# Performance work log

Hardware: AMD Instinct MI355X
Metric: run time of the kernel (lower is better)

Reference implementation:

```python
import jax, jax.numpy as jnp
import numpy as np

B, N, S, K, D = 16, 4096, 1024, 32, 64
MLP = (64, 64, 128)
EPS = 1e-5  # BatchNorm2d default eps


def setup_inputs() -> dict:
    key = jax.random.key(0)
    ks = jax.random.split(key, 16)
    inp = {
        'xyz': jax.random.normal(ks[0], (B, N, 3), dtype=jnp.float32),
        'normals': jax.random.normal(ks[1], (B, N, 3), dtype=jnp.float32),
        'points': jax.random.normal(ks[2], (B, N, D), dtype=jnp.float32),
        'fps_idx': jax.random.randint(ks[3], (B, S), 0, N),
    }
    last = D
    for i, c in enumerate(MLP):
        inp[f'w{i}'] = jax.random.normal(ks[4 + i], (c, last), dtype=jnp.float32) * (1.0 / np.sqrt(last))
        inp[f'b{i}'] = jnp.zeros((c,), dtype=jnp.float32)
        inp[f'g{i}'] = jnp.ones((c,), dtype=jnp.float32)
        inp[f'bt{i}'] = jnp.zeros((c,), dtype=jnp.float32)
        last = c
    return inp


def _group(points, idx):
    # points: [B,N,C], idx: [B,S,K] -> [B,S,K,C]
    b, s, k = idx.shape
    flat = idx.reshape(b, s * k)
    g = jnp.take_along_axis(points, flat[:, :, None], axis=1)
    return g.reshape(b, s, k, points.shape[-1])


def _forward(xyz, normals, points, fps_idx, params):
    new_xyz = jnp.take_along_axis(xyz, fps_idx[:, :, None], axis=1)        # [B,S,3]
    new_normals = jnp.take_along_axis(normals, fps_idx[:, :, None], axis=1)
    # squared distances [B,S,N] (algebraic form of the broadcasted cdist)
    d = (jnp.sum(new_xyz ** 2, -1)[:, :, None]
         + jnp.sum(xyz ** 2, -1)[:, None, :]
         - 2.0 * jnp.einsum('bsc,bnc->bsn', new_xyz, xyz))
    _, idx = jax.lax.top_k(-d, K)                                          # K nearest
    x = _group(points, idx)                                                # [B,S,K,D]
    x = jnp.transpose(x, (0, 3, 2, 1))                                     # [B,D,K,S]
    for (w, b, g, bt) in params:
        x = jnp.einsum('oc,bcks->boks', w, x) + b[None, :, None, None]     # 1x1 conv
        m = jnp.mean(x, axis=(0, 2, 3), keepdims=True)                     # BN (batch stats)
        v = jnp.var(x, axis=(0, 2, 3), keepdims=True)
        x = (x - m) * jax.lax.rsqrt(v + EPS) * g[None, :, None, None] + bt[None, :, None, None]
        x = jax.nn.relu(x)
    feat = jnp.transpose(jnp.max(x, axis=2), (0, 2, 1))                    # [B,S,C_out]
    return new_xyz, new_normals, feat, fps_idx


def reference(xyz, normals, points, fps_idx,
              w0, b0, g0, bt0, w1, b1, g1, bt1, w2, b2, g2, bt2):
    params = ((w0, b0, g0, bt0), (w1, b1, g1, bt1), (w2, b2, g2, bt2))
    return _forward(xyz, normals, points, fps_idx, params)
```

## Files before the change

kernel.cpp:

```cpp
#include <hip/hip_runtime.h>
#include <hip/hip_bf16.h>

#define B_ 16
#define N_ 4096
#define S_ 1024
#define K_ 32
#define D_ 64
#define M_ (B_*S_*K_)
#define EPS_ 1e-5f

#define OUT_NRM  (B_*S_*3)
#define OUT_FEAT (2*B_*S_*3)
#define OUT_FPS  (OUT_FEAT + B_*S_*128)

typedef __attribute__((ext_vector_type(8))) short bf16x8;
typedef __attribute__((ext_vector_type(4))) float f32x4;
typedef unsigned long long u64;

__device__ __forceinline__ unsigned short rnb(float x){
  return (unsigned short)((__float_as_uint(x) + 0x8000u) >> 16);
}
__device__ __forceinline__ void split1(float x, short& h, short& l){
  unsigned ux = __float_as_uint(x);
  unsigned uh = (ux + 0x8000u) & 0xFFFF0000u;
  h = (short)(uh >> 16);
  float lo = x - __uint_as_float(uh);
  l = (short)((__float_as_uint(lo) + 0x8000u) >> 16);
}
__device__ __forceinline__ unsigned f2key(float d){
  unsigned u = __float_as_uint(d);
  return u ^ ((unsigned)(((int)u) >> 31) | 0x80000000u);
}
__device__ __forceinline__ float key2f(unsigned u){
  unsigned v = (u & 0x80000000u) ? (u ^ 0x80000000u) : ~u;
  return __uint_as_float(v);
}
__device__ __forceinline__ unsigned mprefix(u64 m){
  return __builtin_amdgcn_mbcnt_hi((unsigned)(m >> 32),
         __builtin_amdgcn_mbcnt_lo((unsigned)m, 0u));
}

__device__ __forceinline__ float hred4_sum(const float v[4], int l){
  bool hi8 = (l & 8) != 0;
  float send0 = hi8 ? v[0] : v[2];
  float send1 = hi8 ? v[1] : v[3];
  float r0 = __shfl_xor(send0, 8);
  float r1 = __shfl_xor(send1, 8);
  float a0 = (hi8 ? v[2] : v[0]) + r0;
  float a1 = (hi8 ? v[3] : v[1]) + r1;
  bool hi4 = (l & 4) != 0;
  float send = hi4 ? a0 : a1;
  float r = __shfl_xor(send, 4);
  float a = (hi4 ? a1 : a0) + r;
  a += __shfl_xor(a, 2);
  a += __shfl_xor(a, 1);
  return a;
}
__device__ __forceinline__ float hred4_max(const float v[4], int l){
  bool hi8 = (l & 8) != 0;
  float send0 = hi8 ? v[0] : v[2];
  float send1 = hi8 ? v[1] : v[3];
  float r0 = __shfl_xor(send0, 8);
  float r1 = __shfl_xor(send1, 8);
  float a0 = fmaxf(hi8 ? v[2] : v[0], r0);
  float a1 = fmaxf(hi8 ? v[3] : v[1], r1);
  bool hi4 = (l & 4) != 0;
  float send = hi4 ? a0 : a1;
  float r = __shfl_xor(send, 4);
  float a = fmaxf(hi4 ? a1 : a0, r);
  a = fmaxf(a, __shfl_xor(a, 2));
  a = fmaxf(a, __shfl_xor(a, 1));
  return a;
}

__global__ void prep_kernel(const float* __restrict__ xyz, const float* __restrict__ nrm,
                            const int* __restrict__ fps,
                            const float* __restrict__ w0, const float* __restrict__ w1,
                            const float* __restrict__ w2,
                            float* __restrict__ out, float4* __restrict__ px,
                            unsigned short* __restrict__ wdst, float* __restrict__ stats){
  const int bid = blockIdx.x, tid = threadIdx.x;
  if (bid < 256){
    int t = bid*256 + tid;
    const float* p = xyz + (size_t)t*3;
    float x = p[0], y = p[1], z = p[2];
    float pp = __fadd_rn(__fadd_rn(__fmul_rn(x,x), __fmul_rn(y,y)), __fmul_rn(z,z));
    px[t] = make_float4(x, y, z, pp);
  } else if (bid < 320){
    int t = (bid-256)*256 + tid;
    int b = t >> 10;
    int n = fps[t];
    const float* xp = xyz + ((size_t)b*N_ + n)*3;
    out[t*3+0] = xp[0]; out[t*3+1] = xp[1]; out[t*3+2] = xp[2];
    const float* pp = nrm + ((size_t)b*N_ + n)*3;
    out[OUT_NRM + t*3+0] = pp[0]; out[OUT_NRM + t*3+1] = pp[1]; out[OUT_NRM + t*3+2] = pp[2];
    out[OUT_FPS + t] = (float)n;
  } else if (bid < 384){
    int e = (bid-320)*256 + tid;
    const float* W; int base;
    if (e < 4096){ W = w0; base = 0; }
    else if (e < 8192){ W = w1; base = 4096; }
    else { W = w2; base = 8192; }
    int r = e - base;
    int frag = r >> 9;
    int lane = (r >> 3) & 63;
    int j = r & 7;
    int cht = frag >> 1, ks = frag & 1;
    int m = lane & 15, quad = lane >> 4;
    int ch = cht*16 + m, k = ks*32 + quad*8 + j;
    wdst[e] = rnb(W[ch*64 + k]);
  } else {
    stats[(bid-384)*256 + tid] = 0.f;
  }
}

#define DIST3(Q,P) __fsub_rn(__fadd_rn((Q).w,(P).w), __fmul_rn(2.f, \
  __fadd_rn(__fadd_rn(__fmul_rn((Q).x,(P).x), __fmul_rn((Q).y,(P).y)), __fmul_rn((Q).z,(P).z))))

#define RANKSTEP(KK,LO,HI) do{ \
  unsigned mid_ = (LO) + (((HI) - (LO)) >> 1); \
  u64 mm_ = __ballot((KK) <= mid_); \
  if (__popcll(mm_) >= 32) (HI) = mid_; else (LO) = mid_ + 1; \
}while(0)

#define SELFIN(KEY,PAIR,KV,OB) do{ \
  u64 mlt_ = __ballot((KEY) < (KV)); \
  int c1_ = __popcll(mlt_); \
  u64 meq_ = __ballot((KEY) == (KV)); \
  int need_ = 32 - c1_; \
  bool ineq_ = ((KEY) == (KV)); \
  bool seleq_; \
  if (__popcll(meq_) == need_){ seleq_ = ineq_; } \
  else { \
    unsigned myi_ = ineq_ ? (unsigned)((PAIR) & 0xFFFull) : 0xFFFFu; \
    unsigned li_ = 0, hii_ = 0xFFFu; \
    for (int it2_ = 0; it2_ < 12; ++it2_){ \
      unsigned mid_ = li_ + ((hii_ - li_) >> 1); \
      int c_ = __popcll(__ballot(myi_ <= mid_)); \
      if (c_ >= need_) hii_ = mid_; else li_ = mid_ + 1; \
    } \
    seleq_ = (myi_ <= li_); \
  } \
  if ((KEY) < (KV)) idxout[(OB) + mprefix(mlt_)] = (int)((PAIR) & 0xFFFull); \
  u64 msel_ = __ballot(seleq_); \
  if (seleq_) idxout[(OB) + c1_ + mprefix(msel_)] = (int)((PAIR) & 0xFFFull); \
}while(0)

__device__ __forceinline__ void sel_fallback(const u64* sp, unsigned tot, int l,
                                             int* __restrict__ outp){
  if (tot <= 64){
    u64 pair = sp[l];
    u64 plo = 0, phi = (1ull << 44) - 1;
    for (int it = 0; it < 44; ++it){
      u64 mid = plo + ((phi - plo) >> 1);
      u64 m = __ballot(pair <= mid);
      if (__popcll(m) >= 32) phi = mid; else plo = mid + 1;
    }
    bool sel = (pair <= plo);
    u64 m = __ballot(sel);
    unsigned pos = mprefix(m);
    if (sel) outp[pos] = (int)(pair & 0xFFFull);
  } else {
    u64 pa = sp[l], pb = sp[64 + l];
    u64 plo = 0, phi = (1ull << 44) - 1;
    for (int it = 0; it < 44; ++it){
      u64 mid = plo + ((phi - plo) >> 1);
      int c = __popcll(__ballot(pa <= mid)) + __popcll(__ballot(pb <= mid));
      if (c >= 32) phi = mid; else plo = mid + 1;
    }
    int ca = (pa <= plo) ? 1 : 0;
    int cb = (pb <= plo) ? 1 : 0;
    int c2 = ca + cb, inc = c2;
    #pragma unroll
    for (int off = 1; off < 64; off <<= 1){
      int tv = __shfl_up(inc, off);
      if (l >= off) inc += tv;
    }
    int pos = inc - c2;
    if (ca){ outp[pos] = (int)(pa & 0xFFFull); pos++; }
    if (cb){ outp[pos] = (int)(pb & 0xFFFull); }
  }
}

__global__ __launch_bounds__(256, 8) void knn_kernel(const float4* __restrict__ pxyz,
                                                     const int* __restrict__ fps,
                                                     int* __restrict__ idxout){
  __shared__ u64 spair[4][2][128];
  __shared__ float4 stab[256];
  const int t = threadIdx.x, w = t >> 6, l = t & 63;
  const int b = blockIdx.x >> 7;
  const float4* __restrict__ Pp = pxyz + (size_t)b*N_;
  const int q0 = blockIdx.x*8 + w*2;
  const int nq0 = fps[q0], nq1 = fps[q0+1];
  const float4 Q0 = Pp[nq0], Q1 = Pp[nq1];

  float vmin0 = 3.0e38f, vmin1 = 3.0e38f;
  for (int ch = 0; ch < 16; ch++){
    __syncthreads();
    stab[t] = Pp[ch*256 + t];
    __syncthreads();
    #pragma unroll
    for (int j = 0; j < 4; j++){
      float4 P = stab[j*64 + l];
      float d0 = DIST3(Q0, P); vmin0 = fminf(vmin0, d0);
      float d1 = DIST3(Q1, P); vmin1 = fminf(vmin1, d1);
    }
  }

  unsigned a0 = f2key(vmin0), a1 = f2key(vmin1);
  unsigned tl0 = 0, th0 = 0xFFFFFFFFu, tl1 = 0, th1 = 0xFFFFFFFFu;
  for (int it = 0; it < 32; ++it){
    RANKSTEP(a0, tl0, th0);
    RANKSTEP(a1, tl1, th1);
  }
  const float T0 = key2f(tl0), T1 = key2f(tl1);

  spair[w][0][l] = ~0ull; spair[w][0][64 + l] = ~0ull;
  spair[w][1][l] = ~0ull; spair[w][1][64 + l] = ~0ull;

  unsigned cnt0 = 0, cnt1 = 0;
  for (int ch = 0; ch < 16; ch++){
    __syncthreads();
    stab[t] = Pp[ch*256 + t];
    __syncthreads();
    #pragma unroll
    for (int j = 0; j < 4; j++){
      unsigned n = (unsigned)(ch*256 + j*64 + l);
      float4 P = stab[j*64 + l];
      {
        float d = DIST3(Q0, P);
        bool c = (d <= T0);
        u64 m = __ballot(c);
        if (c){ unsigned pos = cnt0 + mprefix(m);
                if (pos < 128) spair[w][0][pos] = ((u64)f2key(d) << 12) | n; }
        cnt0 += (unsigned)__popcll(m);
      }
      {
        float d = DIST3(Q1, P);
        bool c = (d <= T1);
        u64 m = __ballot(c);
        if (c){ unsigned pos = cnt1 + mprefix(m);
                if (pos < 128) spair[w][1][pos] = ((u64)f2key(d) << 12) | n; }
        cnt1 += (unsigned)__popcll(m);
      }
    }
  }

  const size_t obase = (size_t)q0 * K_;
  if (cnt0 <= 64 && cnt1 <= 64){
    u64 P0 = spair[w][0][l], P1 = spair[w][1][l];
    unsigned K0 = (unsigned)(P0 >> 12), K1 = (unsigned)(P1 >> 12);
    unsigned s0l = 0, s0h = 0xFFFFFFFFu, s1l = 0, s1h = 0xFFFFFFFFu;
    for (int it = 0; it < 32; ++it){
      RANKSTEP(K0, s0l, s0h);
      RANKSTEP(K1, s1l, s1h);
    }
    SELFIN(K0, P0, s0l, obase);
    SELFIN(K1, P1, s1l, obase + K_);
  } else {
    sel_fallback(&spair[w][0][0], cnt0, l, idxout + obase);
    sel_fallback(&spair[w][1][0], cnt1, l, idxout + obase + K_);
  }
}

__global__ __launch_bounds__(256, 3) void conv1_mfma(const float* __restrict__ pts,
    const int* __restrict__ idx, const unsigned short* __restrict__ wpk,
    const float* __restrict__ bias, unsigned short* __restrict__ Yo,
    float* __restrict__ stats){
  __shared__ float sred[4][128];
  __shared__ uint4 Wl4[512];
  const unsigned short* Wl = (const unsigned short*)Wl4;
  const int t = threadIdx.x, w = t>>6, l = t&63, quad = l>>4, lr = l&15;
  const int m0 = blockIdx.x*256;
  const int Rw = m0 + w*64;
  const int b = m0 >> 15;
  Wl4[t] = ((const uint4*)wpk)[t];
  Wl4[256 + t] = ((const uint4*)wpk)[256 + t];
  f32x4 acc[4][4];
  #pragma unroll
  for (int c = 0; c < 4; c++)
    #pragma unroll
    for (int rt = 0; rt < 4; rt++)
      acc[c][rt] = (f32x4){0.f,0.f,0.f,0.f};
  int ri[4];
  #pragma unroll
  for (int rt = 0; rt < 4; rt++) ri[rt] = idx[Rw + rt*16 + lr];
  __syncthreads();
  #pragma unroll
  for (int s = 0; s < 2; s++){
    bf16x8 wfs[4];
    #pragma unroll
    for (int c = 0; c < 4; c++)
      wfs[c] = *(const bf16x8*)(Wl + (((c*2+s)<<6) + l)*8);
    #pragma unroll
    for (int rt = 0; rt < 4; rt++){
      const float* pr = pts + ((size_t)(b*4096 + ri[rt]))*64;
      float4 v0 = *(const float4*)(pr + s*32 + quad*8);
      float4 v1 = *(const float4*)(pr + s*32 + quad*8 + 4);
      float xs[8] = {v0.x,v0.y,v0.z,v0.w,v1.x,v1.y,v1.z,v1.w};
      bf16x8 xh, xl;
      #pragma unroll
      for (int j = 0; j < 8; j++){ short hh, ll; split1(xs[j], hh, ll); xh[j]=hh; xl[j]=ll; }
      #pragma unroll
      for (int c = 0; c < 4; c++){
        acc[c][rt] = __builtin_amdgcn_mfma_f32_16x16x32_bf16(wfs[c], xh, acc[c][rt], 0,0,0);
        acc[c][rt] = __builtin_amdgcn_mfma_f32_16x16x32_bf16(wfs[c], xl, acc[c][rt], 0,0,0);
      }
    }
  }
  const int rtg0 = Rw >> 4;
  #pragma unroll
  for (int c = 0; c < 4; c++){
    float4 bq = *(const float4*)(bias + c*16 + quad*4);
    float bqa[4] = {bq.x, bq.y, bq.z, bq.w};
    float sv[4] = {0,0,0,0}, qv[4] = {0,0,0,0};
    int kb = c*2 + (quad>>1);
    int sub = (quad&1)*4;
    #pragma unroll
    for (int rt = 0; rt < 4; rt++){
      float y[4];
      #pragma unroll
      for (int r = 0; r < 4; r++){
        y[r] = acc[c][rt][r] + bqa[r];
        sv[r] += y[r];
        qv[r] += y[r]*y[r];
      }
      uint2 p;
      p.x = (unsigned)rnb(y[0]) | ((unsigned)rnb(y[1])<<16);
      p.y = (unsigned)rnb(y[2]) | ((unsigned)rnb(y[3])<<16);
      *(uint2*)(Yo + ((((rtg0+rt)*8 + kb)*16 + lr)*8 + sub)) = p;
    }
    float S = hred4_sum(sv, l);
    float Q = hred4_sum(qv, l);
    if ((l & 3) == 0){
      int ch = c*16 + quad*4 + ((l>>3)&1)*2 + ((l>>2)&1);
      sred[w][ch] = S;
      sred[w][64 + ch] = Q;
    }
  }
  __syncthreads();
  if (t < 128){
    float tot = sred[0][t]+sred[1][t]+sred[2][t]+sred[3][t];
    unsafeAtomicAdd(&stats[(blockIdx.x & 7)*512 + t], tot);
  }
}

__global__ __launch_bounds__(256, 3) void conv2_mfma(const unsigned short* __restrict__ Yi,
    const unsigned short* __restrict__ wpk, const float* __restrict__ bias,
    const float* __restrict__ gg, const float* __restrict__ btv,
    unsigned short* __restrict__ Yo, float* __restrict__ stats){
  __shared__ float sred[4][128];
  __shared__ float sAff[128];
  __shared__ uint4 Wl4[512];
  const unsigned short* Wl = (const unsigned short*)Wl4;
  const int t = threadIdx.x, w = t>>6, l = t&63, quad = l>>4, lr = l&15;
  const int m0 = blockIdx.x*256;
  const int Rw = m0 + w*64;
  Wl4[t] = ((const uint4*)wpk)[t];
  Wl4[256 + t] = ((const uint4*)wpk)[256 + t];
  if (t < 64){
    const float inv = 1.f/(float)M_;
    float S = 0.f, Q = 0.f;
    #pragma unroll
    for (int r = 0; r < 8; r++){
      S += stats[r*512 + t];
      Q += stats[r*512 + 64 + t];
    }
    float mean = S * inv;
    float var  = Q * inv - mean*mean;
    float a = gg[t] * rsqrtf(var + EPS_);
    sAff[t] = a;
    sAff[64 + t] = btv[t] - mean*a;
  }
  f32x4 acc[4][4];
  #pragma unroll
  for (int c = 0; c < 4; c++)
    #pragma unroll
    for (int rt = 0; rt < 4; rt++)
      acc[c][rt] = (f32x4){0.f,0.f,0.f,0.f};
  const int rtg0 = Rw >> 4;
  uint4 u[2][4];
  #pragma unroll
  for (int s = 0; s < 2; s++)
    #pragma unroll
    for (int rt = 0; rt < 4; rt++)
      u[s][rt] = *(const uint4*)(Yi + (((rtg0+rt)*8 + s*4 + quad)*16 + lr)*8);
  __syncthreads();
  #pragma unroll
  for (int s = 0; s < 2; s++){
    float4 A0 = *(const float4*)(sAff + s*32 + quad*8);
    float4 A1 = *(const float4*)(sAff + s*32 + quad*8 + 4);
    float4 B0 = *(const float4*)(sAff + 64 + s*32 + quad*8);
    float4 B1 = *(const float4*)(sAff + 64 + s*32 + quad*8 + 4);
    float aA[8] = {A0.x,A0.y,A0.z,A0.w,A1.x,A1.y,A1.z,A1.w};
    float aB[8] = {B0.x,B0.y,B0.z,B0.w,B1.x,B1.y,B1.z,B1.w};
    bf16x8 wfs[4];
    #pragma unroll
    for (int c = 0; c < 4; c++)
      wfs[c] = *(const bf16x8*)(Wl + (((c*2+s)<<6) + l)*8);
    #pragma unroll
    for (int rt = 0; rt < 4; rt++){
      unsigned ua[4] = {u[s][rt].x, u[s][rt].y, u[s][rt].z, u[s][rt].w};
      bf16x8 xb;
      #pragma unroll
      for (int j = 0; j < 8; j++){
        unsigned wd = ua[j>>1];
        float yf = __uint_as_float((j&1) ? (wd & 0xFFFF0000u) : (wd << 16));
        float x = fmaxf(0.f, fmaf(yf, aA[j], aB[j]));
        xb[j] = (short)rnb(x);
      }
      #pragma unroll
      for (int c = 0; c < 4; c++)
        acc[c][rt] = __builtin_amdgcn_mfma_f32_16x16x32_bf16(wfs[c], xb, acc[c][rt], 0,0,0);
    }
  }
  #pragma unroll
  for (int c = 0; c < 4; c++){
    float4 bq = *(const float4*)(bias + c*16 + quad*4);
    float bqa[4] = {bq.x, bq.y, bq.z, bq.w};
    float sv[4] = {0,0,0,0}, qv[4] = {0,0,0,0};
    int kb = c*2 + (quad>>1);
    int sub = (quad&1)*4;
    #pragma unroll
    for (int rt = 0; rt < 4; rt++){
      float y[4];
      #pragma unroll
      for (int r = 0; r < 4; r++){
        y[r] = acc[c][rt][r] + bqa[r];
        sv[r] += y[r];
        qv[r] += y[r]*y[r];
      }
      uint2 p;
      p.x = (unsigned)rnb(y[0]) | ((unsigned)rnb(y[1])<<16);
      p.y = (unsigned)rnb(y[2]) | ((unsigned)rnb(y[3])<<16);
      *(uint2*)(Yo + ((((rtg0+rt)*8 + kb)*16 + lr)*8 + sub)) = p;
    }
    float S = hred4_sum(sv, l);
    float Q = hred4_sum(qv, l);
    if ((l & 3) == 0){
      int ch = c*16 + quad*4 + ((l>>3)&1)*2 + ((l>>2)&1);
      sred[w][ch] = S;
      sred[w][64 + ch] = Q;
    }
  }
  __syncthreads();
  if (t < 128){
    float tot = sred[0][t]+sred[1][t]+sred[2][t]+sred[3][t];
    unsafeAtomicAdd(&stats[(blockIdx.x & 7)*512 + 128 + t], tot);
  }
}

__global__ __launch_bounds__(256, 3) void conv3_mfma(const unsigned short* __restrict__ Yi,
    const unsigned short* __restrict__ wpk, const float* __restrict__ bias,
    const float* __restrict__ gg, const float* __restrict__ btv,
    float* __restrict__ ymax, float* __restrict__ stats){
  __shared__ float sred[4][256];
  __shared__ float sAff[128];
  __shared__ uint4 Wl4[1024];
  const unsigned short* Wl = (const unsigned short*)Wl4;
  const int t = threadIdx.x, w = t>>6, l = t&63, quad = l>>4, lr = l&15;
  const int m0 = blockIdx.x*128;
  const int Rw = m0 + w*32;
  #pragma unroll
  for (int i = 0; i < 4; i++) Wl4[i*256 + t] = ((const uint4*)wpk)[i*256 + t];
  if (t < 64){
    const float inv = 1.f/(float)M_;
    float S = 0.f, Q = 0.f;
    #pragma unroll
    for (int r = 0; r < 8; r++){
      S += stats[r*512 + 128 + t];
      Q += stats[r*512 + 192 + t];
    }
    float mean = S * inv;
    float var  = Q * inv - mean*mean;
    float a = gg[t] * rsqrtf(var + EPS_);
    sAff[t] = a;
    sAff[64 + t] = btv[t] - mean*a;
  }
  f32x4 acc[8][2];
  #pragma unroll
  for (int c = 0; c < 8; c++){
    acc[c][0] = (f32x4){0.f,0.f,0.f,0.f};
    acc[c][1] = (f32x4){0.f,0.f,0.f,0.f};
  }
  const int rtg0 = Rw >> 4;
  uint4 u[2][2];
  #pragma unroll
  for (int s = 0; s < 2; s++)
    #pragma unroll
    for (int rt = 0; rt < 2; rt++)
      u[s][rt] = *(const uint4*)(Yi + (((rtg0+rt)*8 + s*4 + quad)*16 + lr)*8);
  __syncthreads();
  #pragma unroll
  for (int s = 0; s < 2; s++){
    float4 A0 = *(const float4*)(sAff + s*32 + quad*8);
    float4 A1 = *(const float4*)(sAff + s*32 + quad*8 + 4);
    float4 B0 = *(const float4*)(sAff + 64 + s*32 + quad*8);
    float4 B1 = *(const float4*)(sAff + 64 + s*32 + quad*8 + 4);
    float aA[8] = {A0.x,A0.y,A0.z,A0.w,A1.x,A1.y,A1.z,A1.w};
    float aB[8] = {B0.x,B0.y,B0.z,B0.w,B1.x,B1.y,B1.z,B1.w};
    #pragma unroll
    for (int rt = 0; rt < 2; rt++){
      unsigned ua[4] = {u[s][rt].x, u[s][rt].y, u[s][rt].z, u[s][rt].w};
      bf16x8 xb;
      #pragma unroll
      for (int j = 0; j < 8; j++){
        unsigned wd = ua[j>>1];
        float yf = __uint_as_float((j&1) ? (wd & 0xFFFF0000u) : (wd << 16));
        float x = fmaxf(0.f, fmaf(yf, aA[j], aB[j]));
        xb[j] = (short)rnb(x);
      }
      #pragma unroll
      for (int c = 0; c < 8; c++){
        bf16x8 wfc = *(const bf16x8*)(Wl + (((c*2+s)<<6) + l)*8);
        acc[c][rt] = __builtin_amdgcn_mfma_f32_16x16x32_bf16(wfc, xb, acc[c][rt], 0,0,0);
      }
    }
  }
  const int g = Rw >> 5;
  #pragma unroll
  for (int c = 0; c < 8; c++){
    float4 bq = *(const float4*)(bias + c*16 + quad*4);
    float bqa[4] = {bq.x, bq.y, bq.z, bq.w};
    float sv[4], qv[4], mv[4];
    #pragma unroll
    for (int r = 0; r < 4; r++){
      float y0 = acc[c][0][r] + bqa[r];
      float y1 = acc[c][1][r] + bqa[r];
      sv[r] = y0 + y1;
      qv[r] = y0*y0 + y1*y1;
      mv[r] = fmaxf(y0, y1);
    }
    float S = hred4_sum(sv, l);
    float Q = hred4_sum(qv, l);
    float Mx = hred4_max(mv, l);
    if ((l & 3) == 0){
      int ch = c*16 + quad*4 + ((l>>3)&1)*2 + ((l>>2)&1);
      sred[w][ch] = S;
      sred[w][128 + ch] = Q;
      ymax[(size_t)g*128 + ch] = Mx;
    }
  }
  __syncthreads();
  {
    float tot = sred[0][t]+sred[1][t]+sred[2][t]+sred[3][t];
    unsafeAtomicAdd(&stats[(blockIdx.x & 7)*512 + 256 + t], tot);
  }
}

__global__ void final_kernel(const float* __restrict__ ymax,
                             const float* __restrict__ stats,
                             const float* __restrict__ gg, const float* __restrict__ btv,
                             float* __restrict__ out){
  __shared__ float sA[128], sB[128];
  const int tid = threadIdx.x;
  if (tid < 128){
    const float inv = 1.f/(float)M_;
    float S = 0.f, Q = 0.f;
    #pragma unroll
    for (int r = 0; r < 8; r++){
      S += stats[r*512 + 256 + tid];
      Q += stats[r*512 + 384 + tid];
    }
    float mean = S * inv;
    float var  = Q * inv - mean*mean;
    float a = gg[tid] * rsqrtf(var + EPS_);
    sA[tid] = a;
    sB[tid] = btv[tid] - mean*a;
  }
  __syncthreads();
  const size_t base = ((size_t)blockIdx.x*256 + tid)*8;
  float4 v0 = *(const float4*)(ymax + base);
  float4 v1 = *(const float4*)(ymax + base + 4);
  const int c0 = (int)(base & 127);
  float4 a0 = *(const float4*)(sA + c0);
  float4 a1 = *(const float4*)(sA + c0 + 4);
  float4 b0 = *(const float4*)(sB + c0);
  float4 b1 = *(const float4*)(sB + c0 + 4);
  float4 o0, o1;
  o0.x = fmaxf(0.f, a0.x*v0.x + b0.x); o0.y = fmaxf(0.f, a0.y*v0.y + b0.y);
  o0.z = fmaxf(0.f, a0.z*v0.z + b0.z); o0.w = fmaxf(0.f, a0.w*v0.w + b0.w);
  o1.x = fmaxf(0.f, a1.x*v1.x + b1.x); o1.y = fmaxf(0.f, a1.y*v1.y + b1.y);
  o1.z = fmaxf(0.f, a1.z*v1.z + b1.z); o1.w = fmaxf(0.f, a1.w*v1.w + b1.w);
  *(float4*)(out + OUT_FEAT + base) = o0;
  *(float4*)(out + OUT_FEAT + base + 4) = o1;
}

extern "C" void kernel_launch(void* const* d_in, const int* in_sizes, int n_in,
                              void* d_out, int out_size, void* d_ws, size_t ws_size,
                              hipStream_t stream) {
  const float* xyz = (const float*)d_in[0];
  const float* nrm = (const float*)d_in[1];
  const float* pts = (const float*)d_in[2];
  const int*   fps = (const int*)d_in[3];
  const float* w0  = (const float*)d_in[4];
  const float* b0  = (const float*)d_in[5];
  const float* g0  = (const float*)d_in[6];
  const float* bt0 = (const float*)d_in[7];
  const float* w1  = (const float*)d_in[8];
  const float* b1  = (const float*)d_in[9];
  const float* g1  = (const float*)d_in[10];
  const float* bt1 = (const float*)d_in[11];
  const float* w2  = (const float*)d_in[12];
  const float* b2  = (const float*)d_in[13];
  const float* g2  = (const float*)d_in[14];
  const float* bt2 = (const float*)d_in[15];
  float* out = (float*)d_out;

  char* ws = (char*)d_ws;
  float* stats = (float*)ws;
  int*   idxb  = (int*)(ws + 20480);
  float* ymax  = (float*)(ws + 2117632);
  float4* pxyz = (float4*)(ws + 10506240);
  unsigned short* wpack = (unsigned short*)(ws + 11554816);
  unsigned short* Y1 = (unsigned short*)(ws + 18878464);
  unsigned short* Y2 = (unsigned short*)(ws + 85987328);

  prep_kernel<<<400, 256, 0, stream>>>(xyz, nrm, fps, w0, w1, w2, out, pxyz, wpack, stats);
  knn_kernel<<<2048, 256, 0, stream>>>(pxyz, fps, idxb);
  conv1_mfma<<<2048, 256, 0, stream>>>(pts, idxb, wpack, b0, Y1, stats);
  conv2_mfma<<<2048, 256, 0, stream>>>(Y1, wpack + 4096, b1, g0, bt0, Y2, stats);
  conv3_mfma<<<4096, 256, 0, stream>>>(Y2, wpack + 8192, b2, g1, bt1, ymax, stats);
  final_kernel<<<1024, 256, 0, stream>>>(ymax, stats, g2, bt2, out);
}
```

Measured before the change: 247.3 us.

## Use FMA-based approximate distance filter with margin and direct global loads in KNN

After: 244.0 us. Within noise of the previous version (-1.3%).

```diff
diff --git a/kernel.cpp b/kernel.cpp
--- a/kernel.cpp
+++ b/kernel.cpp
@@ -85,7 +85,7 @@
     const float* p = xyz + (size_t)t*3;
     float x = p[0], y = p[1], z = p[2];
     float pp = __fadd_rn(__fadd_rn(__fmul_rn(x,x), __fmul_rn(y,y)), __fmul_rn(z,z));
-    px[t] = make_float4(x, y, z, pp);
+    px[t] = make_float4(__fmul_rn(-2.f,x), __fmul_rn(-2.f,y), __fmul_rn(-2.f,z), pp);
   } else if (bid < 320){
     int t = (bid-256)*256 + tid;
     int b = t >> 10;
@@ -114,8 +114,16 @@
   }
 }
 
-#define DIST3(Q,P) __fsub_rn(__fadd_rn((Q).w,(P).w), __fmul_rn(2.f, \
-  __fadd_rn(__fadd_rn(__fmul_rn((Q).x,(P).x), __fmul_rn((Q).y,(P).y)), __fmul_rn((Q).z,(P).z))))
+#define DISTA(P,QX,QY,QZ,QQ) __builtin_fmaf((P).x,(QX), \
+  __builtin_fmaf((P).y,(QY), __builtin_fmaf((P).z,(QZ), (P).w + (QQ))))
+
+__device__ __forceinline__ float dist_exact(float4 P, float qx, float qy, float qz, float qq){
+  float px = -0.5f*P.x, py = -0.5f*P.y, pz = -0.5f*P.z;
+  float dt = __fadd_rn(__fadd_rn(__fmul_rn(qx,px), __fmul_rn(qy,py)), __fmul_rn(qz,pz));
+  return __fsub_rn(__fadd_rn(qq,P.w), __fmul_rn(2.f,dt));
+}
+
+#define MARGIN_ 1e-3f
 
 #define RANKSTEP(KK,LO,HI) do{ \
   unsigned mid_ = (LO) + (((HI) - (LO)) >> 1); \
@@ -186,25 +194,21 @@
                                                      const int* __restrict__ fps,
                                                      int* __restrict__ idxout){
   __shared__ u64 spair[4][2][128];
-  __shared__ float4 stab[256];
   const int t = threadIdx.x, w = t >> 6, l = t & 63;
   const int b = blockIdx.x >> 7;
   const float4* __restrict__ Pp = pxyz + (size_t)b*N_;
   const int q0 = blockIdx.x*8 + w*2;
   const int nq0 = fps[q0], nq1 = fps[q0+1];
   const float4 Q0 = Pp[nq0], Q1 = Pp[nq1];
+  const float qx0 = -0.5f*Q0.x, qy0 = -0.5f*Q0.y, qz0 = -0.5f*Q0.z, qq0 = Q0.w;
+  const float qx1 = -0.5f*Q1.x, qy1 = -0.5f*Q1.y, qz1 = -0.5f*Q1.z, qq1 = Q1.w;
 
   float vmin0 = 3.0e38f, vmin1 = 3.0e38f;
-  for (int ch = 0; ch < 16; ch++){
-    __syncthreads();
-    stab[t] = Pp[ch*256 + t];
-    __syncthreads();
-    #pragma unroll
-    for (int j = 0; j < 4; j++){
-      float4 P = stab[j*64 + l];
-      float d0 = DIST3(Q0, P); vmin0 = fminf(vmin0, d0);
-      float d1 = DIST3(Q1, P); vmin1 = fminf(vmin1, d1);
-    }
+  #pragma unroll 8
+  for (int i = 0; i < 64; i++){
+    float4 P = Pp[i*64 + l];
+    float d0 = DISTA(P, qx0, qy0, qz0, qq0); vmin0 = fminf(vmin0, d0);
+    float d1 = DISTA(P, qx1, qy1, qz1, qq1); vmin1 = fminf(vmin1, d1);
   }
 
   unsigned a0 = f2key(vmin0), a1 = f2key(vmin1);
@@ -213,36 +217,37 @@
     RANKSTEP(a0, tl0, th0);
     RANKSTEP(a1, tl1, th1);
   }
-  const float T0 = key2f(tl0), T1 = key2f(tl1);
+  const float Tm0 = key2f(tl0) + MARGIN_, Tm1 = key2f(tl1) + MARGIN_;
 
   spair[w][0][l] = ~0ull; spair[w][0][64 + l] = ~0ull;
   spair[w][1][l] = ~0ull; spair[w][1][64 + l] = ~0ull;
 
   unsigned cnt0 = 0, cnt1 = 0;
-  for (int ch = 0; ch < 16; ch++){
-    __syncthreads();
-    stab[t] = Pp[ch*256 + t];
-    __syncthreads();
-    #pragma unroll
-    for (int j = 0; j < 4; j++){
-      unsigned n = (unsigned)(ch*256 + j*64 + l);
-      float4 P = stab[j*64 + l];
-      {
-        float d = DIST3(Q0, P);
-        bool c = (d <= T0);
-        u64 m = __ballot(c);
-        if (c){ unsigned pos = cnt0 + mprefix(m);
-                if (pos < 128) spair[w][0][pos] = ((u64)f2key(d) << 12) | n; }
-        cnt0 += (unsigned)__popcll(m);
-      }
-      {
-        float d = DIST3(Q1, P);
-        bool c = (d <= T1);
-        u64 m = __ballot(c);
-        if (c){ unsigned pos = cnt1 + mprefix(m);
-                if (pos < 128) spair[w][1][pos] = ((u64)f2key(d) << 12) | n; }
-        cnt1 += (unsigned)__popcll(m);
-      }
+  #pragma unroll 4
+  for (int i = 0; i < 64; i++){
+    unsigned n = (unsigned)(i*64 + l);
+    float4 P = Pp[n];
+    {
+      float da = DISTA(P, qx0, qy0, qz0, qq0);
+      bool c = (da <= Tm0);
+      u64 m = __ballot(c);
+      if (c){
+        float de = dist_exact(P, qx0, qy0, qz0, qq0);
+        unsigned pos = cnt0 + mprefix(m);
+        if (pos < 128) spair[w][0][pos] = ((u64)f2key(de) << 12) | n;
+      }
+      cnt0 += (unsigned)__popcll(m);
+    }
+    {
+      float da = DISTA(P, qx1, qy1, qz1, qq1);
+      bool c = (da <= Tm1);
+      u64 m = __ballot(c);
+      if (c){
+        float de = dist_exact(P, qx1, qy1, qz1, qq1);
+        unsigned pos = cnt1 + mprefix(m);
+        if (pos < 128) spair[w][1][pos] = ((u64)f2key(de) << 12) | n;
+      }
+      cnt1 += (unsigned)__popcll(m);
     }
   }
 
```
